# Kernel optimization log

Measured on AMD Instinct MI355X. Metric: run time of the kernel, lower is better.

Reference implementation:

```python
import jax, jax.numpy as jnp
import numpy as np

N = 50000      # num_nodes
E = 1000000    # graph edges
EP = 400000    # pos/neg link-pred edges
H = 128        # hidden_dim
C = 768        # chemical_dim
L = 2          # num GCN layers


def setup_inputs() -> dict:
    key = jax.random.key(0)
    ks = jax.random.split(key, 12)
    edge_index = jax.random.randint(ks[0], (2, E), 0, N)
    chemistry = jax.random.normal(ks[1], (N, C), jnp.float32)
    pos_edge = jax.random.randint(ks[2], (EP, 2), 0, N)
    neg_edge = jax.random.randint(ks[3], (EP, 2), 0, N)
    smiles_mask = jax.random.uniform(ks[4], (N,), jnp.float32)
    node_emb = jax.random.normal(ks[5], (N, H), jnp.float32) * 0.1
    conv_w = jax.random.normal(ks[6], (L, H, H), jnp.float32) / np.sqrt(H)
    conv_b = jnp.zeros((L, H), jnp.float32)
    chem_w = jax.random.normal(ks[7], (C, H), jnp.float32) / np.sqrt(C)
    chem_b = jnp.zeros((H,), jnp.float32)
    dec_w1 = jax.random.normal(ks[8], (2 * H, H), jnp.float32) / np.sqrt(2 * H)
    dec_b1 = jnp.zeros((H,), jnp.float32)
    dec_w2 = jax.random.normal(ks[9], (H, 1), jnp.float32) / np.sqrt(H)
    dec_b2 = jnp.zeros((1,), jnp.float32)
    return dict(edge_index=edge_index, chemistry=chemistry, pos_edge=pos_edge,
                neg_edge=neg_edge, smiles_mask=smiles_mask, node_emb=node_emb,
                conv_w=conv_w, conv_b=conv_b, chem_w=chem_w, chem_b=chem_b,
                dec_w1=dec_w1, dec_b1=dec_b1, dec_w2=dec_w2, dec_b2=dec_b2)


def reference(edge_index, chemistry, pos_edge, neg_edge, smiles_mask, node_emb,
              conv_w, conv_b, chem_w, chem_b, dec_w1, dec_b1, dec_w2, dec_b2):
    row, col = edge_index[0], edge_index[1]  # src -> dst
    # GCN symmetric normalization (add_self_loops=False)
    deg = jax.ops.segment_sum(jnp.ones((E,), jnp.float32), col, num_segments=N)
    dinv = jnp.where(deg > 0, 1.0 / jnp.sqrt(jnp.maximum(deg, 1.0)), 0.0)
    norm = dinv[row] * dinv[col]  # [E]

    # Encoder: structure-only GCN over learned node embeddings
    z = node_emb
    for l in range(L):
        h = z @ conv_w[l]                       # [N,H]
        msg = h[row] * norm[:, None]            # gather [E,H]
        agg = jax.ops.segment_sum(msg, col, num_segments=N)  # scatter-add
        z = jax.nn.relu(agg + conv_b[l])

    # Chemistry projection, masked by smiles validity
    c = jax.nn.relu(chemistry @ chem_w + chem_b) * smiles_mask[:, None]  # [N,H]

    def decode(edges):
        src, dst = edges[:, 0], edges[:, 1]
        f = jnp.concatenate([z[src] * z[dst], c[src] * c[dst]], axis=-1)  # [Ep,2H]
        hmid = jax.nn.relu(f @ dec_w1 + dec_b1)
        return (hmid @ dec_w2 + dec_b2)[:, 0]

    return decode(pos_edge), decode(neg_edge)
```

## Files before the change

kernel.cpp:

```cpp
#include <hip/hip_runtime.h>
#include <hip/hip_fp16.h>

#define NN 50000
#define NE 1000000
#define NEP 400000
#define HD 128
#define CD 768
#define NB_SCAN 196
#define FSTR 256

typedef _Float16 f16x8 __attribute__((ext_vector_type(8)));
typedef _Float16 f16x2 __attribute__((ext_vector_type(2)));
typedef __fp16 hf16x2 __attribute__((ext_vector_type(2)));
typedef __attribute__((ext_vector_type(4))) float f32x4;

__device__ __forceinline__ unsigned pk2h(float a, float b) {
    hf16x2 p = __builtin_amdgcn_cvt_pkrtz(a, b);
    return __builtin_bit_cast(unsigned, p);
}
__device__ __forceinline__ ushort f2h(float x) {
    return (ushort)(pk2h(x, 0.f) & 0xffffu);
}
__device__ __forceinline__ unsigned h2mul(unsigned a, unsigned b) {
    f16x2 ha = __builtin_bit_cast(f16x2, a);
    f16x2 hb = __builtin_bit_cast(f16x2, b);
    f16x2 r = ha * hb;
    return __builtin_bit_cast(unsigned, r);
}
__device__ __forceinline__ f16x8 pack8h(float4 a0, float4 a1) {
    union { unsigned u[4]; f16x8 v; } r;
    r.u[0] = pk2h(a0.x, a0.y);
    r.u[1] = pk2h(a0.z, a0.w);
    r.u[2] = pk2h(a1.x, a1.y);
    r.u[3] = pk2h(a1.z, a1.w);
    return r.v;
}
__device__ __forceinline__ float2 h2f2(unsigned u) {
    f16x2 h = __builtin_bit_cast(f16x2, u);
    return make_float2((float)h[0], (float)h[1]);
}

__global__ __launch_bounds__(256) void count_kernel(const int* __restrict__ col,
                                                    int* __restrict__ cnt) {
    int i = blockIdx.x * 256 + threadIdx.x;
    if (i < NE) atomicAdd(&cnt[col[i]], 1);
}

__global__ __launch_bounds__(256) void dinv_kernel(const int* __restrict__ cnt,
                                                   float* __restrict__ dinv) {
    int i = blockIdx.x * 256 + threadIdx.x;
    if (i < NN) {
        int d = cnt[i];
        dinv[i] = (d > 0) ? 1.0f / sqrtf((float)d) : 0.0f;
    }
}

__global__ __launch_bounds__(256) void scan1_kernel(const int* __restrict__ cnt,
                                                    int* __restrict__ partial,
                                                    int* __restrict__ bsum) {
    __shared__ int s[256];
    int i = blockIdx.x * 256 + threadIdx.x;
    int v = (i < NN) ? cnt[i] : 0;
    s[threadIdx.x] = v;
    __syncthreads();
    for (int o = 1; o < 256; o <<= 1) {
        int t = (threadIdx.x >= o) ? s[threadIdx.x - o] : 0;
        __syncthreads();
        s[threadIdx.x] += t;
        __syncthreads();
    }
    if (i < NN) partial[i] = s[threadIdx.x] - v;
    if (threadIdx.x == 255) bsum[blockIdx.x] = s[255];
}

__global__ __launch_bounds__(256) void scan2_kernel(int* __restrict__ bsum) {
    __shared__ int s[256];
    int v = (threadIdx.x < NB_SCAN) ? bsum[threadIdx.x] : 0;
    s[threadIdx.x] = v;
    __syncthreads();
    for (int o = 1; o < 256; o <<= 1) {
        int t = (threadIdx.x >= o) ? s[threadIdx.x - o] : 0;
        __syncthreads();
        s[threadIdx.x] += t;
        __syncthreads();
    }
    if (threadIdx.x < NB_SCAN) bsum[threadIdx.x] = s[threadIdx.x] - v;
}

__global__ __launch_bounds__(256) void scan3_kernel(const int* __restrict__ partial,
                                                    const int* __restrict__ bsum,
                                                    int* __restrict__ off,
                                                    int* __restrict__ cursor) {
    int i = blockIdx.x * 256 + threadIdx.x;
    if (i < NN) {
        int o = partial[i] + bsum[blockIdx.x];
        off[i] = o;
        cursor[i] = o;
    }
}

__global__ __launch_bounds__(256) void fill_kernel(const int* __restrict__ row,
                                                   const int* __restrict__ col,
                                                   const float* __restrict__ dinv,
                                                   int* __restrict__ cursor,
                                                   int* __restrict__ csr_idx,
                                                   float* __restrict__ csr_w) {
    int e = blockIdx.x * 256 + threadIdx.x;
    if (e < NE) {
        int c = col[e], r = row[e];
        int slot = atomicAdd(&cursor[c], 1);
        csr_idx[slot] = r;
        csr_w[slot] = dinv[r];
    }
}

__global__ __launch_bounds__(256) void wfrag_kernel(const float* __restrict__ w,
                                                    ushort* __restrict__ wf) {
    int tid = blockIdx.x * 256 + threadIdx.x;
    int ks = tid >> 9, nt = (tid >> 6) & 7, l = tid & 63;
    int kbase = ks * 32 + ((l >> 4) << 3);
    int colq = nt * 16 + (l & 15);
    ushort r[8];
#pragma unroll
    for (int j = 0; j < 8; ++j) r[j] = f2h(w[(size_t)(kbase + j) * HD + colq]);
    *(uint4*)&wf[(size_t)tid * 8] = *(uint4*)r;
}

template <int KS, bool EPI>
__global__ __launch_bounds__(256) void feat_mfma_kernel(const float* __restrict__ A,
                                                        const ushort* __restrict__ wf,
                                                        const float* __restrict__ bias,
                                                        const float* __restrict__ mask,
                                                        ushort* __restrict__ out,
                                                        int ostride, int ooff) {
    __shared__ float At[64][36];
    const int t = threadIdx.x;
    const int w = t >> 6, lane = t & 63;
    const int rowBase = blockIdx.x * 64;
    const int nt0 = w * 2;
    const int K = KS * 32;

    f32x4 acc[4][2] = {};

    for (int ks = 0; ks < KS; ++ks) {
        __syncthreads();
#pragma unroll
        for (int i = 0; i < 2; ++i) {
            int li = t + i * 256;
            int r = li >> 3, c4 = li & 7;
            int grow = rowBase + r;
            float4 v = make_float4(0.f, 0.f, 0.f, 0.f);
            if (grow < NN) v = *(const float4*)&A[(size_t)grow * K + ks * 32 + c4 * 4];
            *(float4*)&At[r][c4 * 4] = v;
        }
        __syncthreads();
        f16x8 bf0 = ((const f16x8*)wf)[(ks * 8 + nt0) * 64 + lane];
        f16x8 bf1 = ((const f16x8*)wf)[(ks * 8 + nt0 + 1) * 64 + lane];
#pragma unroll
        for (int mt = 0; mt < 4; ++mt) {
            int row = mt * 16 + (lane & 15);
            float4 a0 = *(const float4*)&At[row][(lane >> 4) * 8];
            float4 a1 = *(const float4*)&At[row][(lane >> 4) * 8 + 4];
            f16x8 af = pack8h(a0, a1);
            acc[mt][0] = __builtin_amdgcn_mfma_f32_16x16x32_f16(af, bf0, acc[mt][0], 0, 0, 0);
            acc[mt][1] = __builtin_amdgcn_mfma_f32_16x16x32_f16(af, bf1, acc[mt][1], 0, 0, 0);
        }
    }

    const int c0 = lane & 15, rq = lane >> 4;
    float bb0 = EPI ? bias[nt0 * 16 + c0] : 0.f;
    float bb1 = EPI ? bias[nt0 * 16 + 16 + c0] : 0.f;
#pragma unroll
    for (int mt = 0; mt < 4; ++mt) {
#pragma unroll
        for (int reg = 0; reg < 4; ++reg) {
            int grow = rowBase + mt * 16 + rq * 4 + reg;
            if (grow < NN) {
                float v0 = acc[mt][0][reg], v1 = acc[mt][1][reg];
                if (EPI) {
                    float m = mask[grow];
                    v0 = fmaxf(v0 + bb0, 0.f) * m;
                    v1 = fmaxf(v1 + bb1, 0.f) * m;
                }
                out[(size_t)grow * ostride + ooff + nt0 * 16 + c0] = f2h(v0);
                out[(size_t)grow * ostride + ooff + nt0 * 16 + 16 + c0] = f2h(v1);
            }
        }
    }
}

template <bool F16OUT>
__global__ __launch_bounds__(256) void gather_kernel(const int* __restrict__ off,
                                                     const int* __restrict__ cnt,
                                                     const int* __restrict__ csr_idx,
                                                     const float* __restrict__ csr_w,
                                                     const float* __restrict__ dinv,
                                                     const ushort* __restrict__ h,
                                                     const float* __restrict__ bias,
                                                     float* __restrict__ z,
                                                     ushort* __restrict__ zb,
                                                     int ostride) {
    int v = blockIdx.x * 4 + (threadIdx.x >> 6);
    if (v >= NN) return;
    int lane = threadIdx.x & 63;
    int s = off[v];
    int e = s + cnt[v];
    float accx = 0.f, accy = 0.f;
    for (; s + 3 < e; s += 4) {
        int r0 = csr_idx[s], r1 = csr_idx[s + 1], r2 = csr_idx[s + 2], r3 = csr_idx[s + 3];
        float w0 = csr_w[s], w1 = csr_w[s + 1], w2 = csr_w[s + 2], w3 = csr_w[s + 3];
        unsigned u0 = *(const unsigned*)&h[(size_t)r0 * HD + lane * 2];
        unsigned u1 = *(const unsigned*)&h[(size_t)r1 * HD + lane * 2];
        unsigned u2 = *(const unsigned*)&h[(size_t)r2 * HD + lane * 2];
        unsigned u3 = *(const unsigned*)&h[(size_t)r3 * HD + lane * 2];
        float2 f0 = h2f2(u0), f1 = h2f2(u1), f2 = h2f2(u2), f3 = h2f2(u3);
        accx = fmaf(f0.x, w0, accx); accy = fmaf(f0.y, w0, accy);
        accx = fmaf(f1.x, w1, accx); accy = fmaf(f1.y, w1, accy);
        accx = fmaf(f2.x, w2, accx); accy = fmaf(f2.y, w2, accy);
        accx = fmaf(f3.x, w3, accx); accy = fmaf(f3.y, w3, accy);
    }
    for (; s < e; ++s) {
        int r0 = csr_idx[s];
        float w0 = csr_w[s];
        float2 f0 = h2f2(*(const unsigned*)&h[(size_t)r0 * HD + lane * 2]);
        accx = fmaf(f0.x, w0, accx); accy = fmaf(f0.y, w0, accy);
    }
    float dv = dinv[v];
    float2 b = *(const float2*)&bias[lane * 2];
    float ox = fmaxf(fmaf(accx, dv, b.x), 0.f);
    float oy = fmaxf(fmaf(accy, dv, b.y), 0.f);
    if (F16OUT) {
        *(unsigned*)&zb[(size_t)v * ostride + lane * 2] = pk2h(ox, oy);
    } else {
        float2 o; o.x = ox; o.y = oy;
        *(float2*)&z[(size_t)v * HD + lane * 2] = o;
    }
}

__global__ __launch_bounds__(256, 4) void decode_mfma_kernel(const int* __restrict__ pos_edge,
                                                             const int* __restrict__ neg_edge,
                                                             const ushort* __restrict__ feat,
                                                             const ushort* __restrict__ w1f,
                                                             const float* __restrict__ b1,
                                                             const float* __restrict__ w2,
                                                             const float* __restrict__ b2,
                                                             float* __restrict__ out) {
    __shared__ ushort Flds[8 * 4 * 64 * 8];
    __shared__ int sEdge[128];
    __shared__ float part[4][64];
    const int t = threadIdx.x;
    const int w = t >> 6, lane = t & 63;
    const int bid = blockIdx.x;
    const bool isPos = bid < (NEP / 64);
    const int* edges = isPos ? pos_edge : neg_edge;
    const int ebase = (isPos ? bid : bid - NEP / 64) * 64;
    float* op = out + (isPos ? 0 : NEP);

    if (t < 128) sEdge[t] = edges[(size_t)ebase * 2 + t];
    __syncthreads();

    const int seg = t & 31, eslot = t >> 5;
    uint4 avr[8], bvr[8];
#pragma unroll
    for (int it = 0; it < 8; ++it) {
        int e = it * 8 + eslot;
        int s = sEdge[2 * e], dd = sEdge[2 * e + 1];
        avr[it] = *(const uint4*)&feat[(size_t)s * FSTR + seg * 8];
        bvr[it] = *(const uint4*)&feat[(size_t)dd * FSTR + seg * 8];
    }
#pragma unroll
    for (int it = 0; it < 8; ++it) {
        int e = it * 8 + eslot;
        uint4 res;
        res.x = h2mul(avr[it].x, bvr[it].x);
        res.y = h2mul(avr[it].y, bvr[it].y);
        res.z = h2mul(avr[it].z, bvr[it].z);
        res.w = h2mul(avr[it].w, bvr[it].w);
        int ks = seg >> 2;
        int mt = e >> 4;
        int fl = (e & 15) | ((seg & 3) << 4);
        int swz = (seg & 3) | ((ks & 1) << 2);
        ((uint4*)Flds)[(ks * 4 + mt) * 64 + (fl ^ swz)] = res;
    }
    __syncthreads();

    f32x4 acc[4][2] = {};
    const int nt0 = w * 2;
#pragma unroll
    for (int ks = 0; ks < 8; ++ks) {
        f16x8 bf0 = ((const f16x8*)w1f)[(ks * 8 + nt0) * 64 + lane];
        f16x8 bf1 = ((const f16x8*)w1f)[(ks * 8 + nt0 + 1) * 64 + lane];
        const int rswz = ((lane >> 4) & 3) | ((ks & 1) << 2);
#pragma unroll
        for (int mt = 0; mt < 4; ++mt) {
            f16x8 af = ((const f16x8*)Flds)[(ks * 4 + mt) * 64 + (lane ^ rswz)];
            acc[mt][0] = __builtin_amdgcn_mfma_f32_16x16x32_f16(af, bf0, acc[mt][0], 0, 0, 0);
            acc[mt][1] = __builtin_amdgcn_mfma_f32_16x16x32_f16(af, bf1, acc[mt][1], 0, 0, 0);
        }
    }

    const int c0 = lane & 15, rq = lane >> 4;
    float b1v0 = b1[nt0 * 16 + c0], b1v1 = b1[nt0 * 16 + 16 + c0];
    float w2v0 = w2[nt0 * 16 + c0], w2v1 = w2[nt0 * 16 + 16 + c0];
#pragma unroll
    for (int mt = 0; mt < 4; ++mt) {
#pragma unroll
        for (int reg = 0; reg < 4; ++reg) {
            float h0 = fmaxf(acc[mt][0][reg] + b1v0, 0.f);
            float h1 = fmaxf(acc[mt][1][reg] + b1v1, 0.f);
            float p = fmaf(h0, w2v0, h1 * w2v1);
            p += __shfl_xor(p, 1);
            p += __shfl_xor(p, 2);
            p += __shfl_xor(p, 4);
            p += __shfl_xor(p, 8);
            if (c0 == 0) part[w][mt * 16 + rq * 4 + reg] = p;
        }
    }
    __syncthreads();
    if (t < 64) {
        op[ebase + t] = part[0][t] + part[1][t] + part[2][t] + part[3][t] + b2[0];
    }
}

extern "C" void kernel_launch(void* const* d_in, const int* in_sizes, int n_in,
                              void* d_out, int out_size, void* d_ws, size_t ws_size,
                              hipStream_t stream) {
    const int* edge_index = (const int*)d_in[0];
    const float* chemistry = (const float*)d_in[1];
    const int* pos_edge = (const int*)d_in[2];
    const int* neg_edge = (const int*)d_in[3];
    const float* smiles_mask = (const float*)d_in[4];
    const float* node_emb = (const float*)d_in[5];
    const float* conv_w = (const float*)d_in[6];
    const float* conv_b = (const float*)d_in[7];
    const float* chem_w = (const float*)d_in[8];
    const float* chem_b = (const float*)d_in[9];
    const float* dec_w1 = (const float*)d_in[10];
    const float* dec_b1 = (const float*)d_in[11];
    const float* dec_w2 = (const float*)d_in[12];
    const float* dec_b2 = (const float*)d_in[13];
    float* out = (float*)d_out;

    char* ws = (char*)d_ws;
    int* cnt = (int*)(ws + 0);
    float* dinv = (float*)(ws + 204800);
    int* partial = (int*)(ws + 409600);
    int* off = (int*)(ws + 614400);
    int* cursor = (int*)(ws + 819200);
    int* bsum = (int*)(ws + 1024000);
    int* csr_idx = (int*)(ws + 1048576);
    float* csr_w = (float*)(ws + 5242880);
    float* bufZ = (float*)(ws + 9437184);
    ushort* hb = (ushort*)(ws + 35037184);
    ushort* feat = (ushort*)(ws + 47837184);
    ushort* w1f = (ushort*)(ws + 73437184);
    ushort* wcf = (ushort*)(ws + 73502720);
    ushort* wc0f = (ushort*)(ws + 73699328);
    ushort* wc1f = (ushort*)(ws + 73732096);

    const int* e_row = edge_index;
    const int* e_col = edge_index + NE;

    hipMemsetAsync(cnt, 0, (size_t)NN * 4, stream);
    count_kernel<<<(NE + 255) / 256, 256, 0, stream>>>(e_col, cnt);
    dinv_kernel<<<(NN + 255) / 256, 256, 0, stream>>>(cnt, dinv);
    scan1_kernel<<<NB_SCAN, 256, 0, stream>>>(cnt, partial, bsum);
    scan2_kernel<<<1, 256, 0, stream>>>(bsum);
    scan3_kernel<<<NB_SCAN, 256, 0, stream>>>(partial, bsum, off, cursor);
    fill_kernel<<<(NE + 255) / 256, 256, 0, stream>>>(e_row, e_col, dinv, cursor, csr_idx, csr_w);
    wfrag_kernel<<<16, 256, 0, stream>>>(dec_w1, w1f);
    wfrag_kernel<<<48, 256, 0, stream>>>(chem_w, wcf);
    wfrag_kernel<<<8, 256, 0, stream>>>(conv_w, wc0f);
    wfrag_kernel<<<8, 256, 0, stream>>>(conv_w + HD * HD, wc1f);

    const int mmGrid = (NN + 63) / 64;
    const int gaGrid = (NN + 3) / 4;

    feat_mfma_kernel<4, false><<<mmGrid, 256, 0, stream>>>(node_emb, wc0f, nullptr, nullptr, hb, HD, 0);
    gather_kernel<false><<<gaGrid, 256, 0, stream>>>(off, cnt, csr_idx, csr_w, dinv, hb, conv_b, bufZ, nullptr, 0);

    feat_mfma_kernel<4, false><<<mmGrid, 256, 0, stream>>>(bufZ, wc1f, nullptr, nullptr, hb, HD, 0);
    gather_kernel<true><<<gaGrid, 256, 0, stream>>>(off, cnt, csr_idx, csr_w, dinv, hb, conv_b + HD, nullptr, feat, FSTR);

    feat_mfma_kernel<24, true><<<mmGrid, 256, 0, stream>>>(chemistry, wcf, chem_b, smiles_mask, feat, FSTR, HD);

    decode_mfma_kernel<<<2 * (NEP / 64), 256, 0, stream>>>(pos_edge, neg_edge, feat, w1f,
                                                           dec_b1, dec_w2, dec_b2, out);
}
```

Measured before the change: 451.8 us.

## Remove LDS staging in decode; each wave gathers its own 16 edges into MFMA

Restructures the decoder so each wave owns 16 edges and computes all eight output tiles, loading and multiplying the gathered source/destination features directly into MFMA A-fragments. This drops the shared-memory staging buffer, swizzling, and the block-wide barriers and cross-wave partial reduction. In exchange every wave reads the full first-layer weight fragments instead of a quarter, raising weight traffic through the cache. The occupancy hint is also raised from 4 to 6 blocks per unit.

```diff
diff --git a/kernel.cpp b/kernel.cpp
--- a/kernel.cpp
+++ b/kernel.cpp
@@ -38,6 +38,14 @@
 __device__ __forceinline__ float2 h2f2(unsigned u) {
     f16x2 h = __builtin_bit_cast(f16x2, u);
     return make_float2((float)h[0], (float)h[1]);
+}
+__device__ __forceinline__ f16x8 mul8h(uint4 a, uint4 b) {
+    union { unsigned u[4]; f16x8 v; } r;
+    r.u[0] = h2mul(a.x, b.x);
+    r.u[1] = h2mul(a.y, b.y);
+    r.u[2] = h2mul(a.z, b.z);
+    r.u[3] = h2mul(a.w, b.w);
+    return r.v;
 }
 
 __global__ __launch_bounds__(256) void count_kernel(const int* __restrict__ col,
@@ -237,7 +245,7 @@
     }
 }
 
-__global__ __launch_bounds__(256, 4) void decode_mfma_kernel(const int* __restrict__ pos_edge,
+__global__ __launch_bounds__(256, 6) void decode_mfma_kernel(const int* __restrict__ pos_edge,
                                                              const int* __restrict__ neg_edge,
                                                              const ushort* __restrict__ feat,
                                                              const ushort* __restrict__ w1f,
@@ -245,9 +253,6 @@
                                                              const float* __restrict__ w2,
                                                              const float* __restrict__ b2,
                                                              float* __restrict__ out) {
-    __shared__ ushort Flds[8 * 4 * 64 * 8];
-    __shared__ int sEdge[128];
-    __shared__ float part[4][64];
     const int t = threadIdx.x;
     const int w = t >> 6, lane = t & 63;
     const int bid = blockIdx.x;
@@ -256,69 +261,48 @@
     const int ebase = (isPos ? bid : bid - NEP / 64) * 64;
     float* op = out + (isPos ? 0 : NEP);
 
-    if (t < 128) sEdge[t] = edges[(size_t)ebase * 2 + t];
-    __syncthreads();
-
-    const int seg = t & 31, eslot = t >> 5;
-    uint4 avr[8], bvr[8];
-#pragma unroll
-    for (int it = 0; it < 8; ++it) {
-        int e = it * 8 + eslot;
-        int s = sEdge[2 * e], dd = sEdge[2 * e + 1];
-        avr[it] = *(const uint4*)&feat[(size_t)s * FSTR + seg * 8];
-        bvr[it] = *(const uint4*)&feat[(size_t)dd * FSTR + seg * 8];
-    }
-#pragma unroll
-    for (int it = 0; it < 8; ++it) {
-        int e = it * 8 + eslot;
-        uint4 res;
-        res.x = h2mul(avr[it].x, bvr[it].x);
-        res.y = h2mul(avr[it].y, bvr[it].y);
-        res.z = h2mul(avr[it].z, bvr[it].z);
-        res.w = h2mul(avr[it].w, bvr[it].w);
-        int ks = seg >> 2;
-        int mt = e >> 4;
-        int fl = (e & 15) | ((seg & 3) << 4);
-        int swz = (seg & 3) | ((ks & 1) << 2);
-        ((uint4*)Flds)[(ks * 4 + mt) * 64 + (fl ^ swz)] = res;
-    }
-    __syncthreads();
-
-    f32x4 acc[4][2] = {};
-    const int nt0 = w * 2;
+    const int e = w * 16 + (lane & 15);
+    const int seg = lane >> 4;
+    const int eg = ebase + e;
+    const int s = edges[2 * eg];
+    const int dd = edges[2 * eg + 1];
+    const ushort* sp = feat + (size_t)s * FSTR + seg * 8;
+    const ushort* dp = feat + (size_t)dd * FSTR + seg * 8;
+
+    f32x4 acc[8] = {};
 #pragma unroll
     for (int ks = 0; ks < 8; ++ks) {
-        f16x8 bf0 = ((const f16x8*)w1f)[(ks * 8 + nt0) * 64 + lane];
-        f16x8 bf1 = ((const f16x8*)w1f)[(ks * 8 + nt0 + 1) * 64 + lane];
-        const int rswz = ((lane >> 4) & 3) | ((ks & 1) << 2);
-#pragma unroll
-        for (int mt = 0; mt < 4; ++mt) {
-            f16x8 af = ((const f16x8*)Flds)[(ks * 4 + mt) * 64 + (lane ^ rswz)];
-            acc[mt][0] = __builtin_amdgcn_mfma_f32_16x16x32_f16(af, bf0, acc[mt][0], 0, 0, 0);
-            acc[mt][1] = __builtin_amdgcn_mfma_f32_16x16x32_f16(af, bf1, acc[mt][1], 0, 0, 0);
+        uint4 av = *(const uint4*)(sp + ks * 32);
+        uint4 bv = *(const uint4*)(dp + ks * 32);
+        f16x8 af = mul8h(av, bv);
+#pragma unroll
+        for (int nt = 0; nt < 8; ++nt) {
+            f16x8 bf = ((const f16x8*)w1f)[(ks * 8 + nt) * 64 + lane];
+            acc[nt] = __builtin_amdgcn_mfma_f32_16x16x32_f16(af, bf, acc[nt], 0, 0, 0);
         }
     }
 
     const int c0 = lane & 15, rq = lane >> 4;
-    float b1v0 = b1[nt0 * 16 + c0], b1v1 = b1[nt0 * 16 + 16 + c0];
-    float w2v0 = w2[nt0 * 16 + c0], w2v1 = w2[nt0 * 16 + 16 + c0];
-#pragma unroll
-    for (int mt = 0; mt < 4; ++mt) {
+    float p[4] = {0.f, 0.f, 0.f, 0.f};
+#pragma unroll
+    for (int nt = 0; nt < 8; ++nt) {
+        float b1v = b1[nt * 16 + c0];
+        float w2v = w2[nt * 16 + c0];
 #pragma unroll
         for (int reg = 0; reg < 4; ++reg) {
-            float h0 = fmaxf(acc[mt][0][reg] + b1v0, 0.f);
-            float h1 = fmaxf(acc[mt][1][reg] + b1v1, 0.f);
-            float p = fmaf(h0, w2v0, h1 * w2v1);
-            p += __shfl_xor(p, 1);
-            p += __shfl_xor(p, 2);
-            p += __shfl_xor(p, 4);
-            p += __shfl_xor(p, 8);
-            if (c0 == 0) part[w][mt * 16 + rq * 4 + reg] = p;
-        }
-    }
-    __syncthreads();
-    if (t < 64) {
-        op[ebase + t] = part[0][t] + part[1][t] + part[2][t] + part[3][t] + b2[0];
+            float h = fmaxf(acc[nt][reg] + b1v, 0.f);
+            p[reg] = fmaf(h, w2v, p[reg]);
+        }
+    }
+    float b2v = b2[0];
+#pragma unroll
+    for (int reg = 0; reg < 4; ++reg) {
+        float v = p[reg];
+        v += __shfl_xor(v, 1);
+        v += __shfl_xor(v, 2);
+        v += __shfl_xor(v, 4);
+        v += __shfl_xor(v, 8);
+        if (c0 == 0) op[ebase + w * 16 + rq * 4 + reg] = v + b2v;
     }
 }
 
```

New measurement: 505.3 us. 11.8% more time.

## Bucket-sort decode edges by source node and remap blocks per XCD for locality

Applied to the files above, without the earlier changes.

Adds a histogram, scan and permute pass that groups the 800k decode edges into buckets by source node index (256 nodes per bucket). The decode kernel then reads the sorted edges, remaps block IDs so consecutive buckets land on the same XCD, and scatters each result to its original output index. The aim is better L2 reuse of the source feature rows. The sorting passes add three kernel launches and their atomics, and the output writes become scattered. The gather loop is also unrolled to 8 edges, and the decode loads are fused into the multiply loop, which reduces register pressure.

```diff
diff --git a/kernel.cpp b/kernel.cpp
--- a/kernel.cpp
+++ b/kernel.cpp
@@ -8,6 +8,7 @@
 #define CD 768
 #define NB_SCAN 196
 #define FSTR 256
+#define NBKT 196
 
 typedef _Float16 f16x8 __attribute__((ext_vector_type(8)));
 typedef _Float16 f16x2 __attribute__((ext_vector_type(2)));
@@ -111,6 +112,54 @@
         int slot = atomicAdd(&cursor[c], 1);
         csr_idx[slot] = r;
         csr_w[slot] = dinv[r];
+    }
+}
+
+__global__ __launch_bounds__(256) void ehist_kernel(const int* __restrict__ pos,
+                                                    const int* __restrict__ neg,
+                                                    int* __restrict__ bcnt) {
+    __shared__ int h[NBKT];
+    const int t = threadIdx.x;
+    if (t < NBKT) h[t] = 0;
+    __syncthreads();
+    int i = blockIdx.x * 256 + t;
+    if (i < 2 * NEP) {
+        int s = (i < NEP) ? pos[2 * i] : neg[2 * (i - NEP)];
+        atomicAdd(&h[s >> 8], 1);
+    }
+    __syncthreads();
+    if (t < NBKT && h[t]) atomicAdd(&bcnt[t], h[t]);
+}
+
+__global__ __launch_bounds__(256) void escan_kernel(const int* __restrict__ bcnt,
+                                                    int* __restrict__ bcur) {
+    __shared__ int s[256];
+    const int t = threadIdx.x;
+    int v = (t < NBKT) ? bcnt[t] : 0;
+    s[t] = v;
+    __syncthreads();
+    for (int o = 1; o < 256; o <<= 1) {
+        int x = (t >= o) ? s[t - o] : 0;
+        __syncthreads();
+        s[t] += x;
+        __syncthreads();
+    }
+    if (t < NBKT) bcur[t] = s[t] - v;
+}
+
+__global__ __launch_bounds__(256) void epermute_kernel(const int* __restrict__ pos,
+                                                       const int* __restrict__ neg,
+                                                       int* __restrict__ bcur,
+                                                       uint2* __restrict__ sd,
+                                                       int* __restrict__ oidx) {
+    int i = blockIdx.x * 256 + threadIdx.x;
+    if (i < 2 * NEP) {
+        int s, d;
+        if (i < NEP) { s = pos[2 * i]; d = pos[2 * i + 1]; }
+        else { s = neg[2 * (i - NEP)]; d = neg[2 * (i - NEP) + 1]; }
+        int slot = atomicAdd(&bcur[s >> 8], 1);
+        sd[slot] = make_uint2((unsigned)s, (unsigned)d);
+        oidx[slot] = i;
     }
 }
 
@@ -206,18 +255,29 @@
     int s = off[v];
     int e = s + cnt[v];
     float accx = 0.f, accy = 0.f;
-    for (; s + 3 < e; s += 4) {
+    for (; s + 7 < e; s += 8) {
         int r0 = csr_idx[s], r1 = csr_idx[s + 1], r2 = csr_idx[s + 2], r3 = csr_idx[s + 3];
-        float w0 = csr_w[s], w1 = csr_w[s + 1], w2 = csr_w[s + 2], w3 = csr_w[s + 3];
+        int r4 = csr_idx[s + 4], r5 = csr_idx[s + 5], r6 = csr_idx[s + 6], r7 = csr_idx[s + 7];
         unsigned u0 = *(const unsigned*)&h[(size_t)r0 * HD + lane * 2];
         unsigned u1 = *(const unsigned*)&h[(size_t)r1 * HD + lane * 2];
         unsigned u2 = *(const unsigned*)&h[(size_t)r2 * HD + lane * 2];
         unsigned u3 = *(const unsigned*)&h[(size_t)r3 * HD + lane * 2];
+        unsigned u4 = *(const unsigned*)&h[(size_t)r4 * HD + lane * 2];
+        unsigned u5 = *(const unsigned*)&h[(size_t)r5 * HD + lane * 2];
+        unsigned u6 = *(const unsigned*)&h[(size_t)r6 * HD + lane * 2];
+        unsigned u7 = *(const unsigned*)&h[(size_t)r7 * HD + lane * 2];
+        float w0 = csr_w[s], w1 = csr_w[s + 1], w2 = csr_w[s + 2], w3 = csr_w[s + 3];
+        float w4 = csr_w[s + 4], w5 = csr_w[s + 5], w6 = csr_w[s + 6], w7 = csr_w[s + 7];
         float2 f0 = h2f2(u0), f1 = h2f2(u1), f2 = h2f2(u2), f3 = h2f2(u3);
+        float2 f4 = h2f2(u4), f5 = h2f2(u5), f6 = h2f2(u6), f7 = h2f2(u7);
         accx = fmaf(f0.x, w0, accx); accy = fmaf(f0.y, w0, accy);
         accx = fmaf(f1.x, w1, accx); accy = fmaf(f1.y, w1, accy);
         accx = fmaf(f2.x, w2, accx); accy = fmaf(f2.y, w2, accy);
         accx = fmaf(f3.x, w3, accx); accy = fmaf(f3.y, w3, accy);
+        accx = fmaf(f4.x, w4, accx); accy = fmaf(f4.y, w4, accy);
+        accx = fmaf(f5.x, w5, accx); accy = fmaf(f5.y, w5, accy);
+        accx = fmaf(f6.x, w6, accx); accy = fmaf(f6.y, w6, accy);
+        accx = fmaf(f7.x, w7, accx); accy = fmaf(f7.y, w7, accy);
     }
     for (; s < e; ++s) {
         int r0 = csr_idx[s];
@@ -237,8 +297,8 @@
     }
 }
 
-__global__ __launch_bounds__(256, 4) void decode_mfma_kernel(const int* __restrict__ pos_edge,
-                                                             const int* __restrict__ neg_edge,
+__global__ __launch_bounds__(256, 4) void decode_mfma_kernel(const uint2* __restrict__ sedges,
+                                                             const int* __restrict__ soidx,
                                                              const ushort* __restrict__ feat,
                                                              const ushort* __restrict__ w1f,
                                                              const float* __restrict__ b1,
@@ -247,35 +307,34 @@
                                                              float* __restrict__ out) {
     __shared__ ushort Flds[8 * 4 * 64 * 8];
     __shared__ int sEdge[128];
+    __shared__ int sOut[64];
     __shared__ float part[4][64];
     const int t = threadIdx.x;
     const int w = t >> 6, lane = t & 63;
-    const int bid = blockIdx.x;
-    const bool isPos = bid < (NEP / 64);
-    const int* edges = isPos ? pos_edge : neg_edge;
-    const int ebase = (isPos ? bid : bid - NEP / 64) * 64;
-    float* op = out + (isPos ? 0 : NEP);
-
-    if (t < 128) sEdge[t] = edges[(size_t)ebase * 2 + t];
+
+    const int nwg = gridDim.x;
+    const int orig = blockIdx.x;
+    const int q = nwg >> 3, r = nwg & 7;
+    const int xcd = orig & 7, k = orig >> 3;
+    const int wgid = (xcd < r ? xcd * (q + 1) : r * (q + 1) + (xcd - r) * q) + k;
+    const int ebase = wgid * 64;
+
+    if (t < 128) sEdge[t] = ((const int*)sedges)[(size_t)ebase * 2 + t];
+    if (t < 64) sOut[t] = soidx[ebase + t];
     __syncthreads();
 
     const int seg = t & 31, eslot = t >> 5;
-    uint4 avr[8], bvr[8];
 #pragma unroll
     for (int it = 0; it < 8; ++it) {
         int e = it * 8 + eslot;
         int s = sEdge[2 * e], dd = sEdge[2 * e + 1];
-        avr[it] = *(const uint4*)&feat[(size_t)s * FSTR + seg * 8];
-        bvr[it] = *(const uint4*)&feat[(size_t)dd * FSTR + seg * 8];
-    }
-#pragma unroll
-    for (int it = 0; it < 8; ++it) {
-        int e = it * 8 + eslot;
+        uint4 av = *(const uint4*)&feat[(size_t)s * FSTR + seg * 8];
+        uint4 bv = *(const uint4*)&feat[(size_t)dd * FSTR + seg * 8];
         uint4 res;
-        res.x = h2mul(avr[it].x, bvr[it].x);
-        res.y = h2mul(avr[it].y, bvr[it].y);
-        res.z = h2mul(avr[it].z, bvr[it].z);
-        res.w = h2mul(avr[it].w, bvr[it].w);
+        res.x = h2mul(av.x, bv.x);
+        res.y = h2mul(av.y, bv.y);
+        res.z = h2mul(av.z, bv.z);
+        res.w = h2mul(av.w, bv.w);
         int ks = seg >> 2;
         int mt = e >> 4;
         int fl = (e & 15) | ((seg & 3) << 4);
@@ -318,7 +377,7 @@
     }
     __syncthreads();
     if (t < 64) {
-        op[ebase + t] = part[0][t] + part[1][t] + part[2][t] + part[3][t] + b2[0];
+        out[sOut[t]] = part[0][t] + part[1][t] + part[2][t] + part[3][t] + b2[0];
     }
 }
 
@@ -348,6 +407,8 @@
     int* off = (int*)(ws + 614400);
     int* cursor = (int*)(ws + 819200);
     int* bsum = (int*)(ws + 1024000);
+    int* bcnt = (int*)(ws + 1025024);
+    int* bcur = (int*)(ws + 1026048);
     int* csr_idx = (int*)(ws + 1048576);
     float* csr_w = (float*)(ws + 5242880);
     float* bufZ = (float*)(ws + 9437184);
@@ -357,11 +418,14 @@
     ushort* wcf = (ushort*)(ws + 73502720);
     ushort* wc0f = (ushort*)(ws + 73699328);
     ushort* wc1f = (ushort*)(ws + 73732096);
+    uint2* sort_sd = (uint2*)(ws + 35037184);
+    int* sort_oidx = (int*)(ws + 41437184);
 
     const int* e_row = edge_index;
     const int* e_col = edge_index + NE;
 
     hipMemsetAsync(cnt, 0, (size_t)NN * 4, stream);
+    hipMemsetAsync(bcnt, 0, NBKT * 4, stream);
     count_kernel<<<(NE + 255) / 256, 256, 0, stream>>>(e_col, cnt);
     dinv_kernel<<<(NN + 255) / 256, 256, 0, stream>>>(cnt, dinv);
     scan1_kernel<<<NB_SCAN, 256, 0, stream>>>(cnt, partial, bsum);
@@ -382,8 +446,12 @@
     feat_mfma_kernel<4, false><<<mmGrid, 256, 0, stream>>>(bufZ, wc1f, nullptr, nullptr, hb, HD, 0);
     gather_kernel<true><<<gaGrid, 256, 0, stream>>>(off, cnt, csr_idx, csr_w, dinv, hb, conv_b + HD, nullptr, feat, FSTR);
 
+    ehist_kernel<<<(2 * NEP + 255) / 256, 256, 0, stream>>>(pos_edge, neg_edge, bcnt);
+    escan_kernel<<<1, 256, 0, stream>>>(bcnt, bcur);
+    epermute_kernel<<<(2 * NEP + 255) / 256, 256, 0, stream>>>(pos_edge, neg_edge, bcur, sort_sd, sort_oidx);
+
     feat_mfma_kernel<24, true><<<mmGrid, 256, 0, stream>>>(chemistry, wcf, chem_b, smiles_mask, feat, FSTR, HD);
 
-    decode_mfma_kernel<<<2 * (NEP / 64), 256, 0, stream>>>(pos_edge, neg_edge, feat, w1f,
-                                                           dec_b1, dec_w2, dec_b2, out);
-}
+    decode_mfma_kernel<<<2 * NEP / 64, 256, 0, stream>>>(sort_sd, sort_oidx, feat, w1f,
+                                                         dec_b1, dec_w2, dec_b2, out);
+}
```

New measurement: 930.0 us. 2.06x slower.
